# Kernel optimization log

Hardware: AMD Instinct MI355X
Metric: run time of the kernel (lower is better)

The kernel has to match this reference:

```python
import jax, jax.numpy as jnp
import numpy as np

N = 100000          # nodes
E = 3200000         # edges
C_IN = 64
HIDDEN = 64
NUM_CLASSES = 10
NUM_GRAPHS = 256
EPS = 1e-5


def _graph_conv(x, src, dst, w_rel, w_root, b):
    # PyG GraphConv(aggr='mean'): out_i = W_rel * mean_{j->i} x_j + W_root * x_i + b
    msg_sum = jax.ops.segment_sum(x[src], dst, num_segments=N)            # [N, C]
    cnt = jax.ops.segment_sum(jnp.ones((src.shape[0], 1), x.dtype), dst,
                              num_segments=N)                             # [N, 1]
    agg = msg_sum / jnp.maximum(cnt, 1.0)
    return agg @ w_rel + x @ w_root + b


def _batch_norm(x, gamma, beta):
    # PyG BatchNorm in training mode: batch stats over the node dimension
    mean = jnp.mean(x, axis=0)
    var = jnp.var(x, axis=0)
    return (x - mean) * jax.lax.rsqrt(var + EPS) * gamma + beta


def setup_inputs() -> dict:
    key = jax.random.key(0)
    ks = jax.random.split(key, 20)
    x = jax.random.normal(ks[0], (N, C_IN), dtype=jnp.float32)
    edge_index = jax.random.randint(ks[1], (2, E), 0, N, dtype=jnp.int32)
    batch = jnp.sort(jax.random.randint(ks[2], (N,), 0, NUM_GRAPHS, dtype=jnp.int32))

    def lin(k, fan_in, fan_out):
        s = 1.0 / np.sqrt(fan_in)
        return jax.random.uniform(k, (fan_in, fan_out), jnp.float32, -s, s)

    dims = [(C_IN, 16), (16, 32), (32, 32), (32, HIDDEN)]
    params = {}
    ki = 3
    for i, (ci, co) in enumerate(dims, start=1):
        params[f"w_rel{i}"] = lin(ks[ki], ci, co); ki += 1
        params[f"w_root{i}"] = lin(ks[ki], ci, co); ki += 1
        params[f"b{i}"] = jnp.zeros((co,), jnp.float32)
        params[f"g{i}"] = jnp.ones((co,), jnp.float32)
        params[f"be{i}"] = jnp.zeros((co,), jnp.float32)
    params["w_lin1"] = lin(ks[ki], HIDDEN, HIDDEN); ki += 1
    params["b_lin1"] = jnp.zeros((HIDDEN,), jnp.float32)
    params["w_lin2"] = lin(ks[ki], HIDDEN, NUM_CLASSES); ki += 1
    params["b_lin2"] = jnp.zeros((NUM_CLASSES,), jnp.float32)

    return {"x": x, "edge_index": edge_index, "batch": batch, **params}


def reference(x, edge_index, batch,
              w_rel1, w_root1, b1, g1, be1,
              w_rel2, w_root2, b2, g2, be2,
              w_rel3, w_root3, b3, g3, be3,
              w_rel4, w_root4, b4, g4, be4,
              w_lin1, b_lin1, w_lin2, b_lin2):
    src, dst = edge_index[0], edge_index[1]
    h = jax.nn.elu(_batch_norm(_graph_conv(x, src, dst, w_rel1, w_root1, b1), g1, be1))
    h = jax.nn.elu(_batch_norm(_graph_conv(h, src, dst, w_rel2, w_root2, b2), g2, be2))
    h = jax.nn.elu(_batch_norm(_graph_conv(h, src, dst, w_rel3, w_root3, b3), g3, be3))
    h = jax.nn.elu(_batch_norm(_graph_conv(h, src, dst, w_rel4, w_root4, b4), g4, be4))
    # global mean pool over graphs
    pooled = jax.ops.segment_sum(h, batch, num_segments=NUM_GRAPHS)
    cnt = jax.ops.segment_sum(jnp.ones((N, 1), h.dtype), batch, num_segments=NUM_GRAPHS)
    pooled = pooled / jnp.maximum(cnt, 1.0)
    z = jax.nn.relu(pooled @ w_lin1 + b_lin1)
    # dropout omitted (deterministic / eval mode)
    logits = z @ w_lin2 + b_lin2
    return jax.nn.log_softmax(logits, axis=-1)
```

## Files before the change

kernel.cpp:

```cpp
#include <hip/hip_runtime.h>
#include <hip/hip_bf16.h>
#include <math.h>

#define NGRAPHS 256
#define BSHIFT 8
#define NBUCK 512
#define NSORT 256
#define GCHUNK 1024
#define SMASK 0x00FFFFFFu

__device__ __forceinline__ float bf2f(unsigned short u) {
    return __uint_as_float((unsigned)u << 16);
}
__device__ __forceinline__ unsigned short f2bf(float f) {
    unsigned u = __float_as_uint(f);
    unsigned r = (u + 0x7FFFu + ((u >> 16) & 1u)) >> 16;
    return (unsigned short)r;
}

__global__ __launch_bounds__(256) void k_bhist(const int* __restrict__ dst, int* __restrict__ hmat, int E,
                                               const float* __restrict__ x, const float* __restrict__ w_rel1,
                                               unsigned short* __restrict__ y1b,
                                               float* __restrict__ zbase, int zwords, int N) {
    int bid = blockIdx.x, tid = threadIdx.x;
    if (bid < NSORT) {
        __shared__ int hist[NBUCK];
        for (int i = tid; i < NBUCK; i += 256) hist[i] = 0;
        __syncthreads();
        int chunk = (E + NSORT - 1) / NSORT;
        int lo = bid * chunk;
        int hi = lo + chunk; if (hi > E) hi = E;
        for (int i = lo + tid; i < hi; i += 256)
            atomicAdd(&hist[__builtin_nontemporal_load(dst + i) >> BSHIFT], 1);
        __syncthreads();
        for (int i = tid; i < NBUCK; i += 256)
            hmat[(size_t)bid * NBUCK + i] = hist[i];
    } else {
        if (bid == NSORT) {
            for (int i = tid; i < zwords; i += 256) zbase[i] = 0.f;
        }
        __shared__ float s_rel[64 * 16];
        for (int i = tid; i < 64 * 16; i += 256) s_rel[i] = w_rel1[i];
        __syncthreads();
        int total = N * 4;
        int nb = gridDim.x - NSORT;
        for (int i = (bid - NSORT) * 256 + tid; i < total; i += nb * 256) {
            int n = i >> 2, c0 = (i & 3) << 2;
            const float4* mp = (const float4*)(x + (size_t)n * 64);
            float4 acc; acc.x = 0.f; acc.y = 0.f; acc.z = 0.f; acc.w = 0.f;
#pragma unroll
            for (int k2 = 0; k2 < 16; k2++) {
                float4 v = mp[k2];
                const float* wr = &s_rel[(k2 * 4) * 16 + c0];
                float4 w0 = *(const float4*)(wr);
                float4 w1 = *(const float4*)(wr + 16);
                float4 w2 = *(const float4*)(wr + 32);
                float4 w3 = *(const float4*)(wr + 48);
                acc.x += v.x * w0.x + v.y * w1.x + v.z * w2.x + v.w * w3.x;
                acc.y += v.x * w0.y + v.y * w1.y + v.z * w2.y + v.w * w3.y;
                acc.z += v.x * w0.z + v.y * w1.z + v.z * w2.z + v.w * w3.z;
                acc.w += v.x * w0.w + v.y * w1.w + v.z * w2.w + v.w * w3.w;
            }
            ushort4 o; o.x = f2bf(acc.x); o.y = f2bf(acc.y); o.z = f2bf(acc.z); o.w = f2bf(acc.w);
            *(ushort4*)(y1b + (size_t)n * 16 + c0) = o;
        }
    }
}

__global__ __launch_bounds__(512) void k_scan(int* __restrict__ hmat, int* __restrict__ bstart) {
    __shared__ int s[512];
    int col = threadIdx.x;
    int run = 0;
#pragma unroll 4
    for (int r = 0; r < NSORT; r++) {
        int v = hmat[(size_t)r * NBUCK + col];
        hmat[(size_t)r * NBUCK + col] = run;
        run += v;
    }
    s[col] = run;
    __syncthreads();
    for (int off = 1; off < 512; off <<= 1) {
        int t = (col >= off) ? s[col - off] : 0;
        __syncthreads();
        s[col] += t;
        __syncthreads();
    }
    bstart[col] = s[col] - run;
    if (col == 511) bstart[NBUCK] = s[511];
}

__global__ __launch_bounds__(256) void k_bscatter(const int* __restrict__ src, const int* __restrict__ dst,
                                                  const int* __restrict__ hmat, const int* __restrict__ bstart,
                                                  unsigned* __restrict__ ebuf, int E) {
    __shared__ int cur[NBUCK];
    for (int i = threadIdx.x; i < NBUCK; i += 256)
        cur[i] = bstart[i] + hmat[(size_t)blockIdx.x * NBUCK + i];
    __syncthreads();
    int chunk = (E + NSORT - 1) / NSORT;
    int lo = blockIdx.x * chunk;
    int hi = lo + chunk; if (hi > E) hi = E;
    for (int i = lo + threadIdx.x; i < hi; i += 256) {
        int d = __builtin_nontemporal_load(dst + i);
        int s = __builtin_nontemporal_load(src + i);
        int p = atomicAdd(&cur[d >> BSHIFT], 1);
        ebuf[p] = (unsigned)s | ((unsigned)(d & 255) << 24);
    }
}

__global__ __launch_bounds__(256) void k_sort2(const unsigned* __restrict__ ebuf, const int* __restrict__ bstart,
                                               int* __restrict__ csr, int* __restrict__ row_start, int N) {
    __shared__ int hist[256];
    __shared__ int sc[256];
    __shared__ int scur[256];
    int b = blockIdx.x;
    int e0 = bstart[b], e1 = bstart[b + 1];
    hist[threadIdx.x] = 0;
    __syncthreads();
    for (int i = e0 + threadIdx.x; i < e1; i += 256)
        atomicAdd(&hist[__builtin_nontemporal_load(ebuf + i) >> 24], 1);
    __syncthreads();
    sc[threadIdx.x] = hist[threadIdx.x];
    __syncthreads();
    for (int off = 1; off < 256; off <<= 1) {
        int t = (threadIdx.x >= off) ? sc[threadIdx.x - off] : 0;
        __syncthreads();
        sc[threadIdx.x] += t;
        __syncthreads();
    }
    {
        int inc = sc[threadIdx.x];
        int ex = inc - hist[threadIdx.x];
        scur[threadIdx.x] = e0 + ex;
        int node = (b << BSHIFT) + threadIdx.x;
        if (node < N) row_start[node] = e0 + ex;
        if (node == N - 1) row_start[N] = e0 + inc;
    }
    __syncthreads();
    for (int i = e0 + threadIdx.x; i < e1; i += 256) {
        unsigned w = __builtin_nontemporal_load(ebuf + i);
        int p = atomicAdd(&scur[w >> 24], 1);
        csr[p] = (int)(w & SMASK);
    }
}

template <int C>
__global__ __launch_bounds__(256) void k_gather(const unsigned short* __restrict__ h,
                                                const int* __restrict__ row_start,
                                                const int* __restrict__ csr, float* __restrict__ agg, int N) {
    constexpr int LPR = C / 4;
    constexpr int EPP = 64 / LPR;
    constexpr int BATCH = 4 * EPP;
    __shared__ int sbuf[GCHUNK];
    int lane = threadIdx.x & 63;
    int w = threadIdx.x >> 6;
    int nb = blockIdx.x * 4;
    int wid = nb + w;
    bool act = wid < N;
    int nb_end = nb + 4; if (nb_end > N) nb_end = N;
    int eb0 = row_start[nb];
    int eb1 = row_start[nb_end];
    int r0 = act ? row_start[wid] : 0;
    int r1 = act ? row_start[wid + 1] : 0;
    int es = lane / LPR;
    int cq = (lane % LPR) * 4;

    float a0 = 0.f, a1 = 0.f, a2 = 0.f, a3 = 0.f;
    for (int base = eb0; base < eb1; base += GCHUNK) {
        int len = eb1 - base; if (len > GCHUNK) len = GCHUNK;
        __syncthreads();
        for (int i = threadIdx.x; i < len; i += 256)
            sbuf[i] = __builtin_nontemporal_load(csr + base + i);
        __syncthreads();
        if (act) {
            int lo = (r0 > base ? r0 : base) - base;
            int hiv = r1 < base + len ? r1 : base + len;
            int hi = hiv - base;
            for (int j0 = lo; j0 < hi; j0 += BATCH) {
                int s[4]; bool p[4];
#pragma unroll
                for (int u = 0; u < 4; u++) {
                    int j = j0 + u * EPP + es;
                    p[u] = j < hi;
                    s[u] = sbuf[p[u] ? j : j0];
                }
                ushort4 v[4];
#pragma unroll
                for (int u = 0; u < 4; u++)
                    v[u] = *(const ushort4*)(h + (size_t)s[u] * C + cq);
#pragma unroll
                for (int u = 0; u < 4; u++) {
                    if (p[u]) {
                        a0 += bf2f(v[u].x); a1 += bf2f(v[u].y);
                        a2 += bf2f(v[u].z); a3 += bf2f(v[u].w);
                    }
                }
            }
        }
    }
#pragma unroll
    for (int off = LPR; off < 64; off <<= 1) {
        a0 += __shfl_xor(a0, off, 64);
        a1 += __shfl_xor(a1, off, 64);
        a2 += __shfl_xor(a2, off, 64);
        a3 += __shfl_xor(a3, off, 64);
    }
    if (act && lane < LPR) {
        int deg = r1 - r0;
        float rec = 1.0f / (float)(deg > 0 ? deg : 1);
        float4 o; o.x = a0 * rec; o.y = a1 * rec; o.z = a2 * rec; o.w = a3 * rec;
        *(float4*)(agg + (size_t)wid * C + cq) = o;
    }
}

template <int CI, int CO, bool HAS_REL, bool ADD_AGG, bool IN_BF16>
__global__ __launch_bounds__(256) void k_lin_stats(const void* __restrict__ hroot_v, const float* __restrict__ hrel,
                                                   const float* __restrict__ w_rel, const float* __restrict__ w_root,
                                                   const float* __restrict__ bias,
                                                   float* __restrict__ out, float* __restrict__ gsl, int N) {
    constexpr int QPR = CO / 4;
    __shared__ float s_rel[HAS_REL ? CI * CO : 1];
    __shared__ float s_root[CI * CO];
    __shared__ float s_b[CO];
    __shared__ float part[4][2 * CO];
    int tid = threadIdx.x;
    if (HAS_REL)
        for (int i = tid; i < CI * CO; i += 256) s_rel[i] = w_rel[i];
    for (int i = tid; i < CI * CO; i += 256) s_root[i] = w_root[i];
    if (tid < CO) s_b[tid] = bias[tid];
    __syncthreads();

    int ngrp = (N + 3) >> 2;
    int total = ngrp * QPR;
    int stride = gridDim.x * 256;
    float s0 = 0, s1 = 0, s2 = 0, s3 = 0, q0 = 0, q1 = 0, q2 = 0, q3 = 0;
    for (int i = blockIdx.x * 256 + tid; i < total; i += stride) {
        int g4 = i / QPR, q = i % QPR, c0 = q * 4;
        int n0 = g4 * 4;
        int nm = N - n0; if (nm > 4) nm = 4;
        float4 bias4 = *(const float4*)&s_b[c0];
        float4 acc[4];
#pragma unroll
        for (int m = 0; m < 4; m++) acc[m] = bias4;
        if (ADD_AGG) {
#pragma unroll
            for (int m = 0; m < 4; m++)
                if (m < nm) {
                    float4 v = ((const float4*)hrel)[(size_t)(n0 + m) * QPR + q];
                    acc[m].x += v.x; acc[m].y += v.y; acc[m].z += v.z; acc[m].w += v.w;
                }
        }
#pragma unroll
        for (int cb = 0; cb < CI / 4; cb++) {
            const float* wr = &s_root[(cb * 4) * CO + c0];
            float4 w0 = *(const float4*)(wr);
            float4 w1 = *(const float4*)(wr + CO);
            float4 w2 = *(const float4*)(wr + 2 * CO);
            float4 w3 = *(const float4*)(wr + 3 * CO);
            float4 e0, e1, e2, e3;
            if (HAS_REL) {
                const float* we = &s_rel[(cb * 4) * CO + c0];
                e0 = *(const float4*)(we);
                e1 = *(const float4*)(we + CO);
                e2 = *(const float4*)(we + 2 * CO);
                e3 = *(const float4*)(we + 3 * CO);
            }
#pragma unroll
            for (int m = 0; m < 4; m++) {
                if (m < nm) {
                    float f0, f1, f2, f3;
                    if (IN_BF16) {
                        ushort4 v = *(const ushort4*)((const unsigned short*)hroot_v + (size_t)(n0 + m) * CI + cb * 4);
                        f0 = bf2f(v.x); f1 = bf2f(v.y); f2 = bf2f(v.z); f3 = bf2f(v.w);
                    } else {
                        float4 v = *(const float4*)((const float*)hroot_v + (size_t)(n0 + m) * CI + cb * 4);
                        f0 = v.x; f1 = v.y; f2 = v.z; f3 = v.w;
                    }
                    acc[m].x += f0 * w0.x + f1 * w1.x + f2 * w2.x + f3 * w3.x;
                    acc[m].y += f0 * w0.y + f1 * w1.y + f2 * w2.y + f3 * w3.y;
                    acc[m].z += f0 * w0.z + f1 * w1.z + f2 * w2.z + f3 * w3.z;
                    acc[m].w += f0 * w0.w + f1 * w1.w + f2 * w2.w + f3 * w3.w;
                    if (HAS_REL) {
                        float4 a = *(const float4*)(hrel + (size_t)(n0 + m) * CI + cb * 4);
                        acc[m].x += a.x * e0.x + a.y * e1.x + a.z * e2.x + a.w * e3.x;
                        acc[m].y += a.x * e0.y + a.y * e1.y + a.z * e2.y + a.w * e3.y;
                        acc[m].z += a.x * e0.z + a.y * e1.z + a.z * e2.z + a.w * e3.z;
                        acc[m].w += a.x * e0.w + a.y * e1.w + a.z * e2.w + a.w * e3.w;
                    }
                }
            }
        }
#pragma unroll
        for (int m = 0; m < 4; m++) {
            if (m < nm) {
                ((float4*)out)[(size_t)(n0 + m) * QPR + q] = acc[m];
                s0 += acc[m].x; q0 += acc[m].x * acc[m].x;
                s1 += acc[m].y; q1 += acc[m].y * acc[m].y;
                s2 += acc[m].z; q2 += acc[m].z * acc[m].z;
                s3 += acc[m].w; q3 += acc[m].w * acc[m].w;
            }
        }
    }
#pragma unroll
    for (int off = QPR; off < 64; off <<= 1) {
        s0 += __shfl_xor(s0, off, 64); q0 += __shfl_xor(q0, off, 64);
        s1 += __shfl_xor(s1, off, 64); q1 += __shfl_xor(q1, off, 64);
        s2 += __shfl_xor(s2, off, 64); q2 += __shfl_xor(q2, off, 64);
        s3 += __shfl_xor(s3, off, 64); q3 += __shfl_xor(q3, off, 64);
    }
    int lane = tid & 63;
    int w = tid >> 6;
    if (lane < QPR) {
        int cq = lane * 4;
        part[w][cq + 0] = s0; part[w][CO + cq + 0] = q0;
        part[w][cq + 1] = s1; part[w][CO + cq + 1] = q1;
        part[w][cq + 2] = s2; part[w][CO + cq + 2] = q2;
        part[w][cq + 3] = s3; part[w][CO + cq + 3] = q3;
    }
    __syncthreads();
    if (tid < 2 * CO) {
        float v = part[0][tid] + part[1][tid] + part[2][tid] + part[3][tid];
        atomicAdd(&gsl[tid], v);
    }
}

template <int CO>
__global__ __launch_bounds__(256) void k_bn_elu(const float* __restrict__ h, const float* __restrict__ gsl,
                                                const float* __restrict__ g, const float* __restrict__ be,
                                                unsigned short* __restrict__ hb, float invN, int N) {
    __shared__ float sc[CO], sh[CO];
    if (threadIdx.x < CO) {
        int c = threadIdx.x;
        float mean = gsl[c] * invN;
        float var = gsl[CO + c] * invN - mean * mean;
        float s = g[c] * rsqrtf(var + 1e-5f);
        sc[c] = s;
        sh[c] = be[c] - mean * s;
    }
    __syncthreads();
    int total = N * (CO / 4);
    int i = blockIdx.x * 256 + threadIdx.x;
    if (i >= total) return;
    float4 v = ((const float4*)h)[i];
    int cq = (i % (CO / 4)) * 4;
    v.x = v.x * sc[cq + 0] + sh[cq + 0];
    v.y = v.y * sc[cq + 1] + sh[cq + 1];
    v.z = v.z * sc[cq + 2] + sh[cq + 2];
    v.w = v.w * sc[cq + 3] + sh[cq + 3];
    v.x = v.x > 0.f ? v.x : expm1f(v.x);
    v.y = v.y > 0.f ? v.y : expm1f(v.y);
    v.z = v.z > 0.f ? v.z : expm1f(v.z);
    v.w = v.w > 0.f ? v.w : expm1f(v.w);
    ushort4 o;
    o.x = f2bf(v.x); o.y = f2bf(v.y); o.z = f2bf(v.z); o.w = f2bf(v.w);
    ((ushort4*)hb)[i] = o;
}

__global__ __launch_bounds__(256) void k_bn_elu_pool(const float* __restrict__ h, const float* __restrict__ gsl,
                                                     const float* __restrict__ g, const float* __restrict__ be,
                                                     const int* __restrict__ batch,
                                                     float* __restrict__ pooled, float* __restrict__ cntg,
                                                     float invN, int N) {
    __shared__ float sc[64], sh[64];
    if (threadIdx.x < 64) {
        int c = threadIdx.x;
        float mean = gsl[c] * invN;
        float var = gsl[64 + c] * invN - mean * mean;
        float s = g[c] * rsqrtf(var + 1e-5f);
        sc[c] = s;
        sh[c] = be[c] - mean * s;
    }
    __syncthreads();
    int lane = threadIdx.x & 63;
    int wid = blockIdx.x * 4 + (threadIdx.x >> 6);
    int n0 = wid * 16;
    if (n0 >= N) return;
    float scl = sc[lane];
    float shl = sh[lane];
    int nmax = N - n0; if (nmax > 16) nmax = 16;
    int cur = batch[n0];
    float acc = 0.f;
    float run = 0.f;
    for (int k = 0; k < nmax; k++) {
        int gg = batch[n0 + k];
        if (gg != cur) {
            atomicAdd(&pooled[(size_t)cur * 64 + lane], acc);
            if (lane == 0) atomicAdd(&cntg[cur], run);
            cur = gg; acc = 0.f; run = 0.f;
        }
        float v = h[(size_t)(n0 + k) * 64 + lane] * scl + shl;
        v = v > 0.f ? v : expm1f(v);
        acc += v;
        run += 1.f;
    }
    atomicAdd(&pooled[(size_t)cur * 64 + lane], acc);
    if (lane == 0) atomicAdd(&cntg[cur], run);
}

__global__ __launch_bounds__(256) void k_head(const float* __restrict__ pooled, const float* __restrict__ cntg,
                                              const float* __restrict__ w1, const float* __restrict__ b1,
                                              const float* __restrict__ w2, const float* __restrict__ b2,
                                              float* __restrict__ out) {
    int g = threadIdx.x;
    float rec = 1.0f / fmaxf(cntg[g], 1.0f);
    float p[64];
    {
        const float4* pp = (const float4*)(pooled + (size_t)g * 64);
#pragma unroll
        for (int i = 0; i < 16; i++) {
            float4 v = pp[i];
            p[4 * i + 0] = v.x * rec; p[4 * i + 1] = v.y * rec;
            p[4 * i + 2] = v.z * rec; p[4 * i + 3] = v.w * rec;
        }
    }
    float lg[10];
#pragma unroll
    for (int t = 0; t < 10; t++) lg[t] = b2[t];
#pragma unroll 1
    for (int j = 0; j < 64; j++) {
        float a = b1[j];
#pragma unroll
        for (int k = 0; k < 64; k++) a += p[k] * w1[k * 64 + j];
        a = fmaxf(a, 0.f);
#pragma unroll
        for (int t = 0; t < 10; t++) lg[t] += a * w2[j * 10 + t];
    }
    float m = -1e30f;
#pragma unroll
    for (int t = 0; t < 10; t++) m = fmaxf(m, lg[t]);
    float s = 0.f;
#pragma unroll
    for (int t = 0; t < 10; t++) s += expf(lg[t] - m);
    float lse = m + logf(s);
#pragma unroll
    for (int t = 0; t < 10; t++) out[(size_t)g * 10 + t] = lg[t] - lse;
}

extern "C" void kernel_launch(void* const* d_in, const int* in_sizes, int n_in,
                              void* d_out, int out_size, void* d_ws, size_t ws_size,
                              hipStream_t stream) {
    const float* x = (const float*)d_in[0];
    const int* ei = (const int*)d_in[1];
    const int* batch = (const int*)d_in[2];
    const int N = in_sizes[0] / 64;
    const int E = in_sizes[1] / 2;
    const int* src = ei;
    const int* dst = ei + E;

    const float* w_rel1 = (const float*)d_in[3];
    const float* w_root1 = (const float*)d_in[4];
    const float* b1 = (const float*)d_in[5];
    const float* g1 = (const float*)d_in[6];
    const float* be1 = (const float*)d_in[7];
    const float* w_rel2 = (const float*)d_in[8];
    const float* w_root2 = (const float*)d_in[9];
    const float* b2 = (const float*)d_in[10];
    const float* g2 = (const float*)d_in[11];
    const float* be2 = (const float*)d_in[12];
    const float* w_rel3 = (const float*)d_in[13];
    const float* w_root3 = (const float*)d_in[14];
    const float* b3 = (const float*)d_in[15];
    const float* g3 = (const float*)d_in[16];
    const float* be3 = (const float*)d_in[17];
    const float* w_rel4 = (const float*)d_in[18];
    const float* w_root4 = (const float*)d_in[19];
    const float* b4 = (const float*)d_in[20];
    const float* g4 = (const float*)d_in[21];
    const float* be4 = (const float*)d_in[22];
    const float* w_lin1 = (const float*)d_in[23];
    const float* b_lin1 = (const float*)d_in[24];
    const float* w_lin2 = (const float*)d_in[25];
    const float* b_lin2 = (const float*)d_in[26];

    char* ws = (char*)d_ws;
    size_t off = 0;
    auto alloc = [&](size_t bytes) { size_t o = off; off += (bytes + 255) & ~(size_t)255; return o; };
    int* hmat = (int*)(ws + alloc((size_t)NSORT * NBUCK * 4));
    int* bstart = (int*)(ws + alloc((size_t)(NBUCK + 1) * 4));
    unsigned* ebuf = (unsigned*)(ws + alloc((size_t)E * 4));
    int* csr = (int*)(ws + alloc((size_t)E * 4));
    int* row_start = (int*)(ws + alloc((size_t)(N + 1) * 4));
    float* agg = (float*)(ws + alloc((size_t)N * 32 * 4));
    unsigned short* y1b = (unsigned short*)(ws + alloc((size_t)N * 16 * 2));
    unsigned short* hb = (unsigned short*)(ws + alloc((size_t)N * 64 * 2));
    float* bufA = (float*)(ws + alloc((size_t)N * 64 * 4));
    float* gs = (float*)(ws + alloc((size_t)(512 + NGRAPHS * 64 + NGRAPHS) * 4));
    float* pooled = gs + 512;
    float* cntg = pooled + NGRAPHS * 64;
    const int zwords = 512 + NGRAPHS * 64 + NGRAPHS;

    const float invN = 1.0f / (float)N;
    const int gbl = (N + 3) / 4;
    const int ngrp = (N + 3) / 4;
    auto lsgrid = [&](int qpr) { return (ngrp * qpr + 255) / 256; };

    k_bhist<<<1024, 256, 0, stream>>>(dst, hmat, E, x, w_rel1, y1b, gs, zwords, N);
    k_scan<<<1, 512, 0, stream>>>(hmat, bstart);
    k_bscatter<<<NSORT, 256, 0, stream>>>(src, dst, hmat, bstart, ebuf, E);
    k_sort2<<<NBUCK, 256, 0, stream>>>(ebuf, bstart, csr, row_start, N);

    k_gather<16><<<gbl, 256, 0, stream>>>(y1b, row_start, csr, agg, N);
    k_lin_stats<64, 16, false, true, false><<<lsgrid(4), 256, 0, stream>>>(
        x, agg, nullptr, w_root1, b1, bufA, gs + 0, N);
    k_bn_elu<16><<<(N * 4 + 255) / 256, 256, 0, stream>>>(bufA, gs + 0, g1, be1, hb, invN, N);

    k_gather<16><<<gbl, 256, 0, stream>>>(hb, row_start, csr, agg, N);
    k_lin_stats<16, 32, true, false, true><<<lsgrid(8), 256, 0, stream>>>(
        hb, agg, w_rel2, w_root2, b2, bufA, gs + 128, N);
    k_bn_elu<32><<<(N * 8 + 255) / 256, 256, 0, stream>>>(bufA, gs + 128, g2, be2, hb, invN, N);

    k_gather<32><<<gbl, 256, 0, stream>>>(hb, row_start, csr, agg, N);
    k_lin_stats<32, 32, true, false, true><<<lsgrid(8), 256, 0, stream>>>(
        hb, agg, w_rel3, w_root3, b3, bufA, gs + 256, N);
    k_bn_elu<32><<<(N * 8 + 255) / 256, 256, 0, stream>>>(bufA, gs + 256, g3, be3, hb, invN, N);

    k_gather<32><<<gbl, 256, 0, stream>>>(hb, row_start, csr, agg, N);
    k_lin_stats<32, 64, true, false, true><<<lsgrid(16), 256, 0, stream>>>(
        hb, agg, w_rel4, w_root4, b4, bufA, gs + 384, N);
    int waves16 = (N + 15) / 16;
    k_bn_elu_pool<<<(waves16 + 3) / 4, 256, 0, stream>>>(
        bufA, gs + 384, g4, be4, batch, pooled, cntg, invN, N);

    k_head<<<1, 256, 0, stream>>>(pooled, cntg, w_lin1, b_lin1, w_lin2, b_lin2, (float*)d_out);
}
```

Before: 657.0 us.

## Replace scan kernel with atomic column offsets and fold bucket scan into scatter

The histogram kernel now claims per-block bucket offsets with global atomics on a zeroed column counter, which removes the single-block serial scan kernel. Each scatter block recomputes the 512-entry exclusive scan in shared memory and runs with 512 threads. Zeroing moves to a hipMemsetAsync. Separately, lin_stats now gives each thread four nodes strided by N/4 rather than four consecutive nodes, and drops the grid-stride loop. The atomic offsets make bucket placement nondeterministic, which is fine because sort2 re-sorts within each bucket. The price is redundant scan work in every scatter block and an extra memset launch.

```diff
diff --git a/kernel.cpp b/kernel.cpp
--- a/kernel.cpp
+++ b/kernel.cpp
@@ -21,7 +21,7 @@
 __global__ __launch_bounds__(256) void k_bhist(const int* __restrict__ dst, int* __restrict__ hmat, int E,
                                                const float* __restrict__ x, const float* __restrict__ w_rel1,
                                                unsigned short* __restrict__ y1b,
-                                               float* __restrict__ zbase, int zwords, int N) {
+                                               int* __restrict__ colpos, int N) {
     int bid = blockIdx.x, tid = threadIdx.x;
     if (bid < NSORT) {
         __shared__ int hist[NBUCK];
@@ -33,12 +33,12 @@
         for (int i = lo + tid; i < hi; i += 256)
             atomicAdd(&hist[__builtin_nontemporal_load(dst + i) >> BSHIFT], 1);
         __syncthreads();
-        for (int i = tid; i < NBUCK; i += 256)
-            hmat[(size_t)bid * NBUCK + i] = hist[i];
+        for (int i = tid; i < NBUCK; i += 256) {
+            int h = hist[i];
+            int base = atomicAdd(&colpos[i], h);
+            hmat[(size_t)bid * NBUCK + i] = base;
+        }
     } else {
-        if (bid == NSORT) {
-            for (int i = tid; i < zwords; i += 256) zbase[i] = 0.f;
-        }
         __shared__ float s_rel[64 * 16];
         for (int i = tid; i < 64 * 16; i += 256) s_rel[i] = w_rel1[i];
         __syncthreads();
@@ -67,43 +67,38 @@
     }
 }
 
-__global__ __launch_bounds__(512) void k_scan(int* __restrict__ hmat, int* __restrict__ bstart) {
-    __shared__ int s[512];
-    int col = threadIdx.x;
-    int run = 0;
-#pragma unroll 4
-    for (int r = 0; r < NSORT; r++) {
-        int v = hmat[(size_t)r * NBUCK + col];
-        hmat[(size_t)r * NBUCK + col] = run;
-        run += v;
-    }
-    s[col] = run;
-    __syncthreads();
-    for (int off = 1; off < 512; off <<= 1) {
-        int t = (col >= off) ? s[col - off] : 0;
-        __syncthreads();
-        s[col] += t;
-        __syncthreads();
-    }
-    bstart[col] = s[col] - run;
-    if (col == 511) bstart[NBUCK] = s[511];
-}
-
-__global__ __launch_bounds__(256) void k_bscatter(const int* __restrict__ src, const int* __restrict__ dst,
-                                                  const int* __restrict__ hmat, const int* __restrict__ bstart,
+__global__ __launch_bounds__(512) void k_bscatter(const int* __restrict__ src, const int* __restrict__ dst,
+                                                  const int* __restrict__ hmat, const int* __restrict__ colpos,
+                                                  int* __restrict__ bstart_g,
                                                   unsigned* __restrict__ ebuf, int E) {
+    __shared__ int s[NBUCK];
     __shared__ int cur[NBUCK];
-    for (int i = threadIdx.x; i < NBUCK; i += 256)
-        cur[i] = bstart[i] + hmat[(size_t)blockIdx.x * NBUCK + i];
+    int tid = threadIdx.x;
+    int b = blockIdx.x;
+    int v = colpos[tid];
+    s[tid] = v;
+    __syncthreads();
+    for (int off = 1; off < NBUCK; off <<= 1) {
+        int t = (tid >= off) ? s[tid - off] : 0;
+        __syncthreads();
+        s[tid] += t;
+        __syncthreads();
+    }
+    int excl = s[tid] - v;
+    if (b == 0) {
+        bstart_g[tid] = excl;
+        if (tid == NBUCK - 1) bstart_g[NBUCK] = s[NBUCK - 1];
+    }
+    cur[tid] = excl + hmat[(size_t)b * NBUCK + tid];
     __syncthreads();
     int chunk = (E + NSORT - 1) / NSORT;
-    int lo = blockIdx.x * chunk;
+    int lo = b * chunk;
     int hi = lo + chunk; if (hi > E) hi = E;
-    for (int i = lo + threadIdx.x; i < hi; i += 256) {
+    for (int i = lo + tid; i < hi; i += 512) {
         int d = __builtin_nontemporal_load(dst + i);
-        int s = __builtin_nontemporal_load(src + i);
+        int sv = __builtin_nontemporal_load(src + i);
         int p = atomicAdd(&cur[d >> BSHIFT], 1);
-        ebuf[p] = (unsigned)s | ((unsigned)(d & 255) << 24);
+        ebuf[p] = (unsigned)sv | ((unsigned)(d & 255) << 24);
     }
 }
 
@@ -229,25 +224,25 @@
     if (tid < CO) s_b[tid] = bias[tid];
     __syncthreads();
 
-    int ngrp = (N + 3) >> 2;
-    int total = ngrp * QPR;
-    int stride = gridDim.x * 256;
+    int nq = (N + 3) >> 2;
+    int totalq = nq * QPR;
     float s0 = 0, s1 = 0, s2 = 0, s3 = 0, q0 = 0, q1 = 0, q2 = 0, q3 = 0;
-    for (int i = blockIdx.x * 256 + tid; i < total; i += stride) {
-        int g4 = i / QPR, q = i % QPR, c0 = q * 4;
-        int n0 = g4 * 4;
-        int nm = N - n0; if (nm > 4) nm = 4;
+    int i = blockIdx.x * 256 + tid;
+    if (i < totalq) {
+        int n0 = i / QPR, q = i % QPR, c0 = q * 4;
+        int n1 = n0 + nq, n2 = n0 + 2 * nq, n3 = n0 + 3 * nq;
+        bool v1 = n1 < N, v2 = n2 < N, v3 = n3 < N;
         float4 bias4 = *(const float4*)&s_b[c0];
-        float4 acc[4];
-#pragma unroll
-        for (int m = 0; m < 4; m++) acc[m] = bias4;
+        float4 acc0 = bias4, acc1 = bias4, acc2 = bias4, acc3 = bias4;
         if (ADD_AGG) {
-#pragma unroll
-            for (int m = 0; m < 4; m++)
-                if (m < nm) {
-                    float4 v = ((const float4*)hrel)[(size_t)(n0 + m) * QPR + q];
-                    acc[m].x += v.x; acc[m].y += v.y; acc[m].z += v.z; acc[m].w += v.w;
-                }
+            float4 v = ((const float4*)hrel)[(size_t)n0 * QPR + q];
+            acc0.x += v.x; acc0.y += v.y; acc0.z += v.z; acc0.w += v.w;
+            if (v1) { float4 t = ((const float4*)hrel)[(size_t)n1 * QPR + q];
+                      acc1.x += t.x; acc1.y += t.y; acc1.z += t.z; acc1.w += t.w; }
+            if (v2) { float4 t = ((const float4*)hrel)[(size_t)n2 * QPR + q];
+                      acc2.x += t.x; acc2.y += t.y; acc2.z += t.z; acc2.w += t.w; }
+            if (v3) { float4 t = ((const float4*)hrel)[(size_t)n3 * QPR + q];
+                      acc3.x += t.x; acc3.y += t.y; acc3.z += t.z; acc3.w += t.w; }
         }
 #pragma unroll
         for (int cb = 0; cb < CI / 4; cb++) {
@@ -264,40 +259,53 @@
                 e2 = *(const float4*)(we + 2 * CO);
                 e3 = *(const float4*)(we + 3 * CO);
             }
-#pragma unroll
-            for (int m = 0; m < 4; m++) {
-                if (m < nm) {
-                    float f0, f1, f2, f3;
-                    if (IN_BF16) {
-                        ushort4 v = *(const ushort4*)((const unsigned short*)hroot_v + (size_t)(n0 + m) * CI + cb * 4);
-                        f0 = bf2f(v.x); f1 = bf2f(v.y); f2 = bf2f(v.z); f3 = bf2f(v.w);
-                    } else {
-                        float4 v = *(const float4*)((const float*)hroot_v + (size_t)(n0 + m) * CI + cb * 4);
-                        f0 = v.x; f1 = v.y; f2 = v.z; f3 = v.w;
-                    }
-                    acc[m].x += f0 * w0.x + f1 * w1.x + f2 * w2.x + f3 * w3.x;
-                    acc[m].y += f0 * w0.y + f1 * w1.y + f2 * w2.y + f3 * w3.y;
-                    acc[m].z += f0 * w0.z + f1 * w1.z + f2 * w2.z + f3 * w3.z;
-                    acc[m].w += f0 * w0.w + f1 * w1.w + f2 * w2.w + f3 * w3.w;
-                    if (HAS_REL) {
-                        float4 a = *(const float4*)(hrel + (size_t)(n0 + m) * CI + cb * 4);
-                        acc[m].x += a.x * e0.x + a.y * e1.x + a.z * e2.x + a.w * e3.x;
-                        acc[m].y += a.x * e0.y + a.y * e1.y + a.z * e2.y + a.w * e3.y;
-                        acc[m].z += a.x * e0.z + a.y * e1.z + a.z * e2.z + a.w * e3.z;
-                        acc[m].w += a.x * e0.w + a.y * e1.w + a.z * e2.w + a.w * e3.w;
-                    }
-                }
+#define LIN_BODY(nk, acck, vk)                                                                        \
+            if (vk) {                                                                                 \
+                float f0, f1, f2, f3;                                                                 \
+                if (IN_BF16) {                                                                        \
+                    ushort4 v = *(const ushort4*)((const unsigned short*)hroot_v + (size_t)(nk) * CI + cb * 4); \
+                    f0 = bf2f(v.x); f1 = bf2f(v.y); f2 = bf2f(v.z); f3 = bf2f(v.w);                   \
+                } else {                                                                              \
+                    float4 v = *(const float4*)((const float*)hroot_v + (size_t)(nk) * CI + cb * 4);  \
+                    f0 = v.x; f1 = v.y; f2 = v.z; f3 = v.w;                                           \
+                }                                                                                     \
+                acck.x += f0 * w0.x + f1 * w1.x + f2 * w2.x + f3 * w3.x;                              \
+                acck.y += f0 * w0.y + f1 * w1.y + f2 * w2.y + f3 * w3.y;                              \
+                acck.z += f0 * w0.z + f1 * w1.z + f2 * w2.z + f3 * w3.z;                              \
+                acck.w += f0 * w0.w + f1 * w1.w + f2 * w2.w + f3 * w3.w;                              \
+                if (HAS_REL) {                                                                        \
+                    float4 a = *(const float4*)(hrel + (size_t)(nk) * CI + cb * 4);                   \
+                    acck.x += a.x * e0.x + a.y * e1.x + a.z * e2.x + a.w * e3.x;                      \
+                    acck.y += a.x * e0.y + a.y * e1.y + a.z * e2.y + a.w * e3.y;                      \
+                    acck.z += a.x * e0.z + a.y * e1.z + a.z * e2.z + a.w * e3.z;                      \
+                    acck.w += a.x * e0.w + a.y * e1.w + a.z * e2.w + a.w * e3.w;                      \
+                }                                                                                     \
             }
-        }
-#pragma unroll
-        for (int m = 0; m < 4; m++) {
-            if (m < nm) {
-                ((float4*)out)[(size_t)(n0 + m) * QPR + q] = acc[m];
-                s0 += acc[m].x; q0 += acc[m].x * acc[m].x;
-                s1 += acc[m].y; q1 += acc[m].y * acc[m].y;
-                s2 += acc[m].z; q2 += acc[m].z * acc[m].z;
-                s3 += acc[m].w; q3 += acc[m].w * acc[m].w;
-            }
+            LIN_BODY(n0, acc0, true)
+            LIN_BODY(n1, acc1, v1)
+            LIN_BODY(n2, acc2, v2)
+            LIN_BODY(n3, acc3, v3)
+#undef LIN_BODY
+        }
+        {
+            ((float4*)out)[(size_t)n0 * QPR + q] = acc0;
+            s0 += acc0.x; q0 += acc0.x * acc0.x; s1 += acc0.y; q1 += acc0.y * acc0.y;
+            s2 += acc0.z; q2 += acc0.z * acc0.z; s3 += acc0.w; q3 += acc0.w * acc0.w;
+        }
+        if (v1) {
+            ((float4*)out)[(size_t)n1 * QPR + q] = acc1;
+            s0 += acc1.x; q0 += acc1.x * acc1.x; s1 += acc1.y; q1 += acc1.y * acc1.y;
+            s2 += acc1.z; q2 += acc1.z * acc1.z; s3 += acc1.w; q3 += acc1.w * acc1.w;
+        }
+        if (v2) {
+            ((float4*)out)[(size_t)n2 * QPR + q] = acc2;
+            s0 += acc2.x; q0 += acc2.x * acc2.x; s1 += acc2.y; q1 += acc2.y * acc2.y;
+            s2 += acc2.z; q2 += acc2.z * acc2.z; s3 += acc2.w; q3 += acc2.w * acc2.w;
+        }
+        if (v3) {
+            ((float4*)out)[(size_t)n3 * QPR + q] = acc3;
+            s0 += acc3.x; q0 += acc3.x * acc3.x; s1 += acc3.y; q1 += acc3.y * acc3.y;
+            s2 += acc3.z; q2 += acc3.z * acc3.z; s3 += acc3.w; q3 += acc3.w * acc3.w;
         }
     }
 #pragma unroll
@@ -483,19 +491,21 @@
     unsigned short* y1b = (unsigned short*)(ws + alloc((size_t)N * 16 * 2));
     unsigned short* hb = (unsigned short*)(ws + alloc((size_t)N * 64 * 2));
     float* bufA = (float*)(ws + alloc((size_t)N * 64 * 4));
-    float* gs = (float*)(ws + alloc((size_t)(512 + NGRAPHS * 64 + NGRAPHS) * 4));
+    const int zwords = NBUCK + 512 + NGRAPHS * 64 + NGRAPHS;
+    int* colpos = (int*)(ws + alloc((size_t)zwords * 4));
+    float* gs = (float*)(colpos + NBUCK);
     float* pooled = gs + 512;
     float* cntg = pooled + NGRAPHS * 64;
-    const int zwords = 512 + NGRAPHS * 64 + NGRAPHS;
+
+    hipMemsetAsync(colpos, 0, (size_t)zwords * 4, stream);
 
     const float invN = 1.0f / (float)N;
     const int gbl = (N + 3) / 4;
-    const int ngrp = (N + 3) / 4;
-    auto lsgrid = [&](int qpr) { return (ngrp * qpr + 255) / 256; };
-
-    k_bhist<<<1024, 256, 0, stream>>>(dst, hmat, E, x, w_rel1, y1b, gs, zwords, N);
-    k_scan<<<1, 512, 0, stream>>>(hmat, bstart);
-    k_bscatter<<<NSORT, 256, 0, stream>>>(src, dst, hmat, bstart, ebuf, E);
+    const int nq = (N + 3) / 4;
+    auto lsgrid = [&](int qpr) { return (nq * qpr + 255) / 256; };
+
+    k_bhist<<<1024, 256, 0, stream>>>(dst, hmat, E, x, w_rel1, y1b, colpos, N);
+    k_bscatter<<<NSORT, 512, 0, stream>>>(src, dst, hmat, colpos, bstart, ebuf, E);
     k_sort2<<<NBUCK, 256, 0, stream>>>(ebuf, bstart, csr, row_start, N);
 
     k_gather<16><<<gbl, 256, 0, stream>>>(y1b, row_start, csr, agg, N);
```

Result: faster. 609.3 us (-7.3%).
